# Optimization experiments

Measured on AMD Instinct MI355X. Metric: run time of the kernel, lower is better.

Reference implementation:

```python
import jax, jax.numpy as jnp
import numpy as np

THRESH = 0.59275  # PercolationQ default threshold
SIZES = list(range(3, 42, 2))  # 20 Chebyshev scales
B, P, C = 16, 100, 3


def _connected_components(imgs):
    # imgs: (N, s, s) int32 in {0,1}. 4-connectivity CC via min-label propagation.
    # Label value = (min flat index in component) + 1, background = 0.
    N, s, _ = imgs.shape
    big = s * s + 1
    fg = imgs > 0
    idx = jnp.arange(s * s, dtype=jnp.int32).reshape(1, s, s) + 1
    init = jnp.where(fg, idx, big)

    def body(state):
        L, _ = state
        Lp = jnp.pad(L, ((0, 0), (1, 1), (1, 1)), constant_values=big)
        m = jnp.minimum(jnp.minimum(Lp[:, :-2, 1:-1], Lp[:, 2:, 1:-1]),
                        jnp.minimum(Lp[:, 1:-1, :-2], Lp[:, 1:-1, 2:]))
        Ln = jnp.where(fg, jnp.minimum(L, m), big)
        return Ln, jnp.any(Ln != L)

    L, _ = jax.lax.while_loop(lambda st: st[1], body, (init, jnp.bool_(True)))
    return jnp.where(fg, L, 0)


def _scale_features(x):
    b, p, s, _, c = x.shape
    # --- Chebyshev layer (faithful to the TF reshape + center-crop semantics) ---
    r = x.reshape(b * s, p, s, c)
    center = r[:, (p - 1) // 2, (s - 1) // 2, :][:, None, None, :]
    binm = (jnp.abs(r - center).max(axis=3) <= float(s)).astype(jnp.int32).reshape(b, p, s, s)
    # --- Probability: histogram of per-patch foreground counts ---
    counts = binm.sum(axis=(2, 3))  # (b, p), values in [0, s^2]
    L = s * s + 1
    hist = jax.vmap(lambda cc: jnp.bincount(cc, length=L))(counts).astype(jnp.float32) / p
    numbers = jnp.concatenate([jnp.ones((1,), jnp.float32), jnp.arange(1, L, dtype=jnp.float32)])
    # --- FractalDimension / Lacunarity ---
    fd = (hist / numbers).sum(axis=1)
    mu1 = (hist * numbers).sum(axis=1) ** 2
    mu2 = (hist * numbers ** 2).sum(axis=1)
    lac = (mu2 - mu1) / mu1
    # --- PercolationQ ---
    pq = ((counts.astype(jnp.float32) / (s * s)) >= THRESH).astype(jnp.float32).mean(axis=1)
    # --- Clusterize (tfa semantics: labels unique/consecutive across the whole batch) ---
    labels = _connected_components(binm.reshape(b * p, s, s))
    lhist = jax.vmap(lambda l: jnp.bincount(l.ravel(), length=L))(labels)  # (b*p, s^2+1)
    ncomp = (lhist[:, 1:] > 0).sum(axis=1)
    # max global label in image i = cumulative component count (0 if no components)
    maxlab = jnp.where(ncomp > 0, jnp.cumsum(ncomp), 0)
    pc = maxlab.astype(jnp.float32).reshape(b, p).mean(axis=1)
    # PercolationM: max bincount over per-sample flattened global labels
    #   = max(total background pixels, largest component size in the sample)
    bg = lhist[:, 0].reshape(b, p).sum(axis=1)
    maxcomp = lhist[:, 1:].max(axis=1).reshape(b, p).max(axis=1)
    pm = jnp.maximum(bg, maxcomp).astype(jnp.float32)
    return fd, lac, pq, pc, pm


def _forward(xs):
    feats = [_scale_features(x) for x in xs]
    fd = jnp.stack([f[0] for f in feats], axis=1)
    lac = jnp.stack([f[1] for f in feats], axis=1)
    pq = jnp.stack([f[2] for f in feats], axis=1)
    pc = jnp.stack([f[3] for f in feats], axis=1)
    pm = jnp.stack([f[4] for f in feats], axis=1)
    out = jnp.concatenate([pc, pq, pm, lac, fd], axis=1)  # (B, 100)
    return out.reshape(-1, 10, 10)


def setup_inputs() -> dict:
    key = jax.random.key(0)
    inp = {}
    for i, s in enumerate(SIZES):
        inp[f"x{i}"] = jax.random.normal(jax.random.fold_in(key, i), (B, P, s, s, C), dtype=jnp.float32)
    return inp


def reference(x0, x1, x2, x3, x4, x5, x6, x7, x8, x9, x10, x11, x12, x13, x14, x15, x16, x17, x18, x19):
    return _forward([x0, x1, x2, x3, x4, x5, x6, x7, x8, x9, x10, x11, x12, x13, x14, x15, x16, x17, x18, x19])
```

## Files before the change

kernel.cpp:

```cpp
#include <hip/hip_runtime.h>

#define NSCALES 20
#define PATCH 100
#define IMGS_PER_SCALE 1600
#define TOTAL_IMGS 32000
#define THREADS 256
#define PXT 16
#define CHUNKPX (THREADS * PXT)
#define MAXIMG 464
#define S2MAX 1681

struct Ptrs   { const float* p[NSCALES]; };
struct Starts { int blkStart[NSCALES]; };

template<int S>
__device__ __forceinline__ void count_body(const float* __restrict__ x,
                                           int blkLocal, int sc,
                                           int* __restrict__ wsC2,
                                           float4* cenL, int* cntL)
{
    constexpr int S2 = S * S;
    constexpr int ROWDIV = 100 * S;
    const int Ntot = IMGS_PER_SCALE * S2;
    const int P0   = blkLocal * CHUNKPX;
    const int Pend = min(P0 + CHUNKPX, Ntot);
    const int tid  = threadIdx.x;

    const int imgBase = P0 / S2;
    const int imgLast = (Pend - 1) / S2;
    const int nImg    = imgLast - imgBase + 1;
    const int j0      = P0 / ROWDIV;
    const int jEnd    = (Pend - 1) / ROWDIV;
    const int nj      = jEnd - j0 + 1;

    if (tid < nj) {
        int j = j0 + tid;
        const float* c = x + (size_t)(((j * PATCH + 49) * S + (S >> 1)) * 3);
        cenL[tid] = make_float4(c[0], c[1], c[2], 0.f);
    }
    for (int t = tid; t < nImg; t += THREADS) cntL[t] = 0;
    __syncthreads();

    const int p0 = P0 + tid * PXT;
    if (p0 < Pend) {
        const float4* q4 = (const float4*)(x + (size_t)p0 * 3);
        float4 v[12];
        #pragma unroll
        for (int q = 0; q < 12; q++) v[q] = q4[q];
        const float* f = (const float*)v;

        const int iA = p0 / S2;
        const int r0 = p0 - iA * S2;
        const int jA = p0 / ROWDIV;
        const int jB = (p0 + PXT - 1) / ROWDIV;
        const float4 ceA = cenL[jA - j0];
        const float4 ceB = (jB != jA) ? cenL[jB - j0] : ceA;
        const int flip = (jB != jA) ? ((jA + 1) * ROWDIV - p0) : PXT;

        int cA = 0, cB = 0, cC = 0;
        #pragma unroll
        for (int q = 0; q < PXT; q++) {
            const float4 ce = (q < flip) ? ceA : ceB;
            float d = fmaxf(fmaxf(fabsf(f[q*3+0] - ce.x),
                                  fabsf(f[q*3+1] - ce.y)),
                            fabsf(f[q*3+2] - ce.z));
            int fg = (d <= (float)S) ? 1 : 0;
            int t  = r0 + q;
            if constexpr (S2 >= PXT) {
                cA += (t < S2) ? fg : 0;
                cB += (t >= S2) ? fg : 0;
            } else {
                cA += (t < S2) ? fg : 0;
                cB += (t >= S2 && t < 2 * S2) ? fg : 0;
                cC += (t >= 2 * S2) ? fg : 0;
            }
        }
        atomicAdd(&cntL[iA - imgBase], cA);
        if (cB) atomicAdd(&cntL[iA + 1 - imgBase], cB);
        if constexpr (S2 < PXT) {
            if (cC) atomicAdd(&cntL[iA + 2 - imgBase], cC);
        }
    }
    __syncthreads();

    for (int t = tid; t < nImg; t += THREADS) {
        int img = imgBase + t;
        int lo = img * S2, hi = lo + S2;
        int g = sc * IMGS_PER_SCALE + img;
        int vv = cntL[t];
        if (lo >= P0) {
            wsC2[2 * g] = vv;
            if (hi <= Pend) wsC2[2 * g + 1] = 0;
        } else {
            wsC2[2 * g + 1] = vv;
        }
    }
}

__global__ __launch_bounds__(THREADS)
void count_kernel(Ptrs ptrs, Starts st, int* __restrict__ wsC2)
{
    const int bid = blockIdx.x;
    int sc = 0;
    #pragma unroll
    for (int k = 1; k < NSCALES; k++) sc += (bid >= st.blkStart[k]) ? 1 : 0;
    const int blkLocal = bid - st.blkStart[sc];

    __shared__ float4 cenL[16];
    __shared__ int    cntL[MAXIMG];

    switch (sc) {
#define CASE(i) case i: count_body<3 + 2*(i)>(ptrs.p[i], blkLocal, i, wsC2, cenL, cntL); break;
        CASE(0)  CASE(1)  CASE(2)  CASE(3)  CASE(4)
        CASE(5)  CASE(6)  CASE(7)  CASE(8)  CASE(9)
        CASE(10) CASE(11) CASE(12) CASE(13) CASE(14)
        CASE(15) CASE(16) CASE(17) CASE(18) CASE(19)
#undef CASE
    }
}

__global__ __launch_bounds__(THREADS)
void cc_kernel(Ptrs ptrs, const int* __restrict__ wsC2,
               int* __restrict__ wsCnt,
               int* __restrict__ wsNcomp, int* __restrict__ wsMaxc)
{
    const int bid = blockIdx.x;
    const int sc  = bid / 25;
    const int s   = 3 + 2 * sc;
    const int s2  = s * s;
    const int BIGL = s2 + 1;
    const float* __restrict__ x = ptrs.p[sc];
    const int imgLoc0 = (bid % 25) * 64;
    const int tid = threadIdx.x;
    const unsigned mS = 0xFFFFFFFFu / (unsigned)s + 1;

    __shared__ int slowList[64];
    __shared__ int nslow;
    __shared__ int lab[S2MAX];
    __shared__ int szh[S2MAX];
    __shared__ int redN[4], redM[4];

    if (tid == 0) nslow = 0;
    __syncthreads();
    if (tid < 64) {
        int img = imgLoc0 + tid;
        int g = sc * IMGS_PER_SCALE + img;
        int c = wsC2[2 * g] + wsC2[2 * g + 1];
        wsCnt[g] = c;
        if (c == s2)      { wsNcomp[g] = 1; wsMaxc[g] = s2; }
        else if (c == 0)  { wsNcomp[g] = 0; wsMaxc[g] = 0; }
        else { int k = atomicAdd(&nslow, 1); slowList[k] = img; }
    }
    __syncthreads();
    const int ns = nslow;
    if (ns == 0) return;

    if (s2 <= 64) {
        const int w = tid >> 6, l = tid & 63;
        for (int idx = w; idx < ns; idx += 4) {
            int img = slowList[idx];
            int fg = 0, labr = BIGL, i1 = 0, i2 = 0;
            if (l < s2) {
                i1 = (int)__umulhi((unsigned)l, mS);
                i2 = l - i1 * s;
                int M = img * s + i1;
                int j = M / PATCH;
                const float* ce = x + (size_t)(((j * PATCH + 49) * s + (s >> 1)) * 3);
                const float* px = x + ((size_t)img * s2 + l) * 3;
                float d = fmaxf(fmaxf(fabsf(px[0] - ce[0]), fabsf(px[1] - ce[1])),
                                fabsf(px[2] - ce[2]));
                if (d <= (float)s) { fg = 1; labr = l + 1; }
            }
            for (;;) {
                int m = labr;
                int vU = __shfl(labr, (l - s) & 63);
                int vD = __shfl(labr, (l + s) & 63);
                int vL = __shfl(labr, (l - 1) & 63);
                int vR = __shfl(labr, (l + 1) & 63);
                if (fg) {
                    if (i1 > 0)     m = min(m, vU);
                    if (i1 < s - 1) m = min(m, vD);
                    if (i2 > 0)     m = min(m, vL);
                    if (i2 < s - 1) m = min(m, vR);
                }
                int vJ = __shfl(labr, (m - 1) & 63);
                if (fg) m = min(m, vJ);
                unsigned long long chg = __ballot(m < labr);
                labr = m;
                if (chg == 0) break;
            }
            int ncomp = __popcll(__ballot(fg && labr == l + 1));
            int mc = 0;
            for (int r = 0; r < s2; r++) {
                int szr = __popcll(__ballot(fg && labr == r + 1));
                mc = max(mc, szr);
            }
            if (l == 0) {
                int g = sc * IMGS_PER_SCALE + img;
                wsNcomp[g] = ncomp; wsMaxc[g] = mc;
            }
        }
    } else {
        for (int idx = 0; idx < ns; idx++) {
            int img = slowList[idx];
            const int ibase = img * s2 * 3;
            for (int i = tid; i < s2; i += THREADS) {
                int i1 = (int)__umulhi((unsigned)i, mS);
                int M = img * s + i1;
                int j = M / PATCH;
                const float* ce = x + (size_t)(((j * PATCH + 49) * s + (s >> 1)) * 3);
                const float* px = x + ibase + i * 3;
                float d = fmaxf(fmaxf(fabsf(px[0] - ce[0]), fabsf(px[1] - ce[1])),
                                fabsf(px[2] - ce[2]));
                lab[i] = (d <= (float)s) ? (i + 1) : BIGL;
                szh[i] = 0;
            }
            __syncthreads();
            for (;;) {
                bool changed = false;
                for (int i = tid; i < s2; i += THREADS) {
                    int L0 = lab[i];
                    if (L0 <= s2) {
                        int i1 = (int)__umulhi((unsigned)i, mS);
                        int i2 = i - i1 * s;
                        int m = L0;
                        if (i1 > 0)     m = min(m, lab[i - s]);
                        if (i1 < s - 1) m = min(m, lab[i + s]);
                        if (i2 > 0)     m = min(m, lab[i - 1]);
                        if (i2 < s - 1) m = min(m, lab[i + 1]);
                        m = min(m, lab[m - 1]);
                        if (m < L0) { lab[i] = m; changed = true; }
                    }
                }
                if (__syncthreads_count(changed ? 1 : 0) == 0) break;
            }
            int ncomp = 0;
            for (int i = tid; i < s2; i += THREADS) {
                int L = lab[i];
                if (L <= s2) {
                    atomicAdd(&szh[L - 1], 1);
                    if (L == i + 1) ncomp++;
                }
            }
            __syncthreads();
            int mc = 0;
            for (int i = tid; i < s2; i += THREADS) mc = max(mc, szh[i]);
            for (int m = 32; m >= 1; m >>= 1) {
                ncomp += __shfl_xor(ncomp, m);
                mc     = max(mc, __shfl_xor(mc, m));
            }
            int wid = tid >> 6, lane = tid & 63;
            if (lane == 0) { redN[wid] = ncomp; redM[wid] = mc; }
            __syncthreads();
            if (tid == 0) {
                int g = sc * IMGS_PER_SCALE + img;
                wsNcomp[g] = redN[0] + redN[1] + redN[2] + redN[3];
                wsMaxc[g]  = max(max(redM[0], redM[1]), max(redM[2], redM[3]));
            }
            __syncthreads();
        }
    }
}

__global__ __launch_bounds__(THREADS)
void final_kernel(const int* __restrict__ wsCnt,
                  const int* __restrict__ wsNcomp,
                  const int* __restrict__ wsMaxc,
                  float* __restrict__ out)
{
    const int scale = blockIdx.x;
    const int s  = 3 + 2 * scale;
    const int s2 = s * s;
    const int tid = threadIdx.x;
    const int NB = IMGS_PER_SCALE;
    const int CH = 7;

    __shared__ int nc[IMGS_PER_SCALE];
    __shared__ int tsum[THREADS];

    for (int i = tid; i < NB; i += THREADS) nc[i] = wsNcomp[scale * NB + i];
    __syncthreads();

    int lsum = 0;
    for (int k = 0; k < CH; k++) {
        int idx = tid * CH + k;
        if (idx < NB) lsum += nc[idx];
    }
    tsum[tid] = lsum;
    __syncthreads();
    for (int st = 1; st < THREADS; st <<= 1) {
        int v = (tid >= st) ? tsum[tid - st] : 0;
        __syncthreads();
        tsum[tid] += v;
        __syncthreads();
    }
    int run = (tid > 0) ? tsum[tid - 1] : 0;
    for (int k = 0; k < CH; k++) {
        int idx = tid * CH + k;
        if (idx < NB) {
            int v = nc[idx];
            run += v;
            nc[idx] = (v > 0) ? run : 0;
        }
    }
    __syncthreads();

    int b    = tid >> 4;
    int lane = tid & 15;
    float fdsum = 0.f, sn = 0.f, sn2 = 0.f, pcsum = 0.f;
    int pqc = 0, bg = 0, mcx = 0;
    for (int q = lane; q < PATCH; q += 16) {
        int i = b * PATCH + q;
        int c = wsCnt[scale * NB + i];
        float n = (c > 0) ? (float)c : 1.0f;
        fdsum += 1.0f / n;
        sn    += n;
        sn2   += n * n;
        pqc   += ((float)c / (float)s2 >= 0.59275f) ? 1 : 0;
        bg    += (s2 - c);
        mcx    = max(mcx, wsMaxc[scale * NB + i]);
        pcsum += (float)nc[i];
    }
    for (int m = 8; m >= 1; m >>= 1) {
        fdsum += __shfl_xor(fdsum, m);
        sn    += __shfl_xor(sn, m);
        sn2   += __shfl_xor(sn2, m);
        pcsum += __shfl_xor(pcsum, m);
        pqc   += __shfl_xor(pqc, m);
        bg    += __shfl_xor(bg, m);
        mcx    = max(mcx, __shfl_xor(mcx, m));
    }
    if (lane == 0) {
        float fd  = fdsum / 100.0f;
        float m1  = sn / 100.0f;
        float mu1 = m1 * m1;
        float mu2 = sn2 / 100.0f;
        float lac = (mu2 - mu1) / mu1;
        float pq  = (float)pqc / 100.0f;
        float pc  = pcsum / 100.0f;
        float pm  = (float)max(bg, mcx);
        out[b * 100 +  0 + scale] = pc;
        out[b * 100 + 20 + scale] = pq;
        out[b * 100 + 40 + scale] = pm;
        out[b * 100 + 60 + scale] = lac;
        out[b * 100 + 80 + scale] = fd;
    }
}

extern "C" void kernel_launch(void* const* d_in, const int* in_sizes, int n_in,
                              void* d_out, int out_size, void* d_ws, size_t ws_size,
                              hipStream_t stream)
{
    Ptrs ptrs;
    for (int i = 0; i < NSCALES; i++) ptrs.p[i] = (const float*)d_in[i];

    Starts st;
    int acc = 0;
    for (int i = 0; i < NSCALES; i++) {
        st.blkStart[i] = acc;
        int s = 3 + 2 * i, s2 = s * s;
        acc += (IMGS_PER_SCALE * s2 + CHUNKPX - 1) / CHUNKPX;
    }

    int* wsC2  = (int*)d_ws;
    int* wsCnt = wsC2 + 2 * TOTAL_IMGS;
    int* wsN   = wsCnt + TOTAL_IMGS;
    int* wsM   = wsN + TOTAL_IMGS;

    count_kernel<<<acc, THREADS, 0, stream>>>(ptrs, st, wsC2);
    cc_kernel<<<TOTAL_IMGS / 64, THREADS, 0, stream>>>(ptrs, wsC2, wsCnt, wsN, wsM);
    final_kernel<<<NSCALES, THREADS, 0, stream>>>(wsCnt, wsN, wsM, (float*)d_out);
}
```

Baseline: 67.68 us.

## Stage count-kernel input through LDS with coalesced float4 loads and smaller chunks

The count kernel now has each thread load float4s in a coalesced, thread-interleaved pattern into a shared-memory staging buffer. Each thread then reads 4 pixels twice from shared memory, replacing the old scheme where a thread read 12 contiguous float4s directly from global memory. The chunk per block is halved to 2048 pixels, which doubles the block count and shrinks the per-block image count buffer. The aim is better global memory coalescing and more parallelism, at the cost of 24KB of LDS per block, an extra staging pass and more per-block overhead.

Measured after the change: 67.63 us. About the same (-0.1%).

```diff
diff --git a/kernel.cpp b/kernel.cpp
--- a/kernel.cpp
+++ b/kernel.cpp
@@ -5,9 +5,10 @@
 #define IMGS_PER_SCALE 1600
 #define TOTAL_IMGS 32000
 #define THREADS 256
-#define PXT 16
-#define CHUNKPX (THREADS * PXT)
-#define MAXIMG 464
+#define CHUNKPX 2048
+#define NF4BLK (CHUNKPX * 3 / 4)
+#define F4PT (NF4BLK / THREADS)
+#define MAXIMG 240
 #define S2MAX 1681
 
 struct Ptrs   { const float* p[NSCALES]; };
@@ -17,14 +18,16 @@
 __device__ __forceinline__ void count_body(const float* __restrict__ x,
                                            int blkLocal, int sc,
                                            int* __restrict__ wsC2,
-                                           float4* cenL, int* cntL)
+                                           float4* stgF4, float4* cenL,
+                                           int* cntL)
 {
     constexpr int S2 = S * S;
     constexpr int ROWDIV = 100 * S;
-    const int Ntot = IMGS_PER_SCALE * S2;
-    const int P0   = blkLocal * CHUNKPX;
-    const int Pend = min(P0 + CHUNKPX, Ntot);
-    const int tid  = threadIdx.x;
+    const int Ntot   = IMGS_PER_SCALE * S2;
+    const int NF4tot = Ntot * 3 / 4;
+    const int P0     = blkLocal * CHUNKPX;
+    const int Pend   = min(P0 + CHUNKPX, Ntot);
+    const int tid    = threadIdx.x;
 
     const int imgBase = P0 / S2;
     const int imgLast = (Pend - 1) / S2;
@@ -33,52 +36,55 @@
     const int jEnd    = (Pend - 1) / ROWDIV;
     const int nj      = jEnd - j0 + 1;
 
+    const float4* __restrict__ x4 = (const float4*)x;
+    const int F0 = blkLocal * NF4BLK;
+    float4 stg[F4PT];
+    #pragma unroll
+    for (int it = 0; it < F4PT; it++) {
+        int fi = F0 + it * THREADS + tid;
+        stg[it] = x4[min(fi, NF4tot - 1)];
+    }
     if (tid < nj) {
         int j = j0 + tid;
         const float* c = x + (size_t)(((j * PATCH + 49) * S + (S >> 1)) * 3);
         cenL[tid] = make_float4(c[0], c[1], c[2], 0.f);
     }
     for (int t = tid; t < nImg; t += THREADS) cntL[t] = 0;
-    __syncthreads();
-
-    const int p0 = P0 + tid * PXT;
-    if (p0 < Pend) {
-        const float4* q4 = (const float4*)(x + (size_t)p0 * 3);
-        float4 v[12];
-        #pragma unroll
-        for (int q = 0; q < 12; q++) v[q] = q4[q];
-        const float* f = (const float*)v;
-
-        const int iA = p0 / S2;
-        const int r0 = p0 - iA * S2;
-        const int jA = p0 / ROWDIV;
-        const int jB = (p0 + PXT - 1) / ROWDIV;
-        const float4 ceA = cenL[jA - j0];
-        const float4 ceB = (jB != jA) ? cenL[jB - j0] : ceA;
-        const int flip = (jB != jA) ? ((jA + 1) * ROWDIV - p0) : PXT;
-
-        int cA = 0, cB = 0, cC = 0;
-        #pragma unroll
-        for (int q = 0; q < PXT; q++) {
-            const float4 ce = (q < flip) ? ceA : ceB;
-            float d = fmaxf(fmaxf(fabsf(f[q*3+0] - ce.x),
-                                  fabsf(f[q*3+1] - ce.y)),
-                            fabsf(f[q*3+2] - ce.z));
-            int fg = (d <= (float)S) ? 1 : 0;
-            int t  = r0 + q;
-            if constexpr (S2 >= PXT) {
+    #pragma unroll
+    for (int it = 0; it < F4PT; it++) stgF4[it * THREADS + tid] = stg[it];
+    __syncthreads();
+
+    const float* lf = (const float*)stgF4;
+    #pragma unroll
+    for (int half = 0; half < 2; half++) {
+        const int p0 = P0 + half * (CHUNKPX / 2) + tid * 4;
+        if (p0 < Pend) {
+            const float4* src = (const float4*)(lf + (size_t)(p0 - P0) * 3);
+            float4 a = src[0], b = src[1], c = src[2];
+            const float f[12] = {a.x,a.y,a.z,a.w, b.x,b.y,b.z,b.w,
+                                 c.x,c.y,c.z,c.w};
+            const int iA = p0 / S2;
+            const int r0 = p0 - iA * S2;
+            const int jA = p0 / ROWDIV;
+            const int jB = (p0 + 3) / ROWDIV;
+            const float4 ceA = cenL[jA - j0];
+            const float4 ceB = (jB != jA) ? cenL[jB - j0] : ceA;
+            const int flip = (jB != jA) ? ((jA + 1) * ROWDIV - p0) : 4;
+
+            int cA = 0, cB = 0;
+            #pragma unroll
+            for (int q = 0; q < 4; q++) {
+                const float4 ce = (q < flip) ? ceA : ceB;
+                float d = fmaxf(fmaxf(fabsf(f[q*3+0] - ce.x),
+                                      fabsf(f[q*3+1] - ce.y)),
+                                fabsf(f[q*3+2] - ce.z));
+                int fg = (d <= (float)S) ? 1 : 0;
+                int t  = r0 + q;
                 cA += (t < S2) ? fg : 0;
                 cB += (t >= S2) ? fg : 0;
-            } else {
-                cA += (t < S2) ? fg : 0;
-                cB += (t >= S2 && t < 2 * S2) ? fg : 0;
-                cC += (t >= 2 * S2) ? fg : 0;
-            }
-        }
-        atomicAdd(&cntL[iA - imgBase], cA);
-        if (cB) atomicAdd(&cntL[iA + 1 - imgBase], cB);
-        if constexpr (S2 < PXT) {
-            if (cC) atomicAdd(&cntL[iA + 2 - imgBase], cC);
+            }
+            atomicAdd(&cntL[iA - imgBase], cA);
+            if (cB) atomicAdd(&cntL[iA + 1 - imgBase], cB);
         }
     }
     __syncthreads();
@@ -106,11 +112,12 @@
     for (int k = 1; k < NSCALES; k++) sc += (bid >= st.blkStart[k]) ? 1 : 0;
     const int blkLocal = bid - st.blkStart[sc];
 
-    __shared__ float4 cenL[16];
+    __shared__ float4 stgF4[NF4BLK];
+    __shared__ float4 cenL[8];
     __shared__ int    cntL[MAXIMG];
 
     switch (sc) {
-#define CASE(i) case i: count_body<3 + 2*(i)>(ptrs.p[i], blkLocal, i, wsC2, cenL, cntL); break;
+#define CASE(i) case i: count_body<3 + 2*(i)>(ptrs.p[i], blkLocal, i, wsC2, stgF4, cenL, cntL); break;
         CASE(0)  CASE(1)  CASE(2)  CASE(3)  CASE(4)
         CASE(5)  CASE(6)  CASE(7)  CASE(8)  CASE(9)
         CASE(10) CASE(11) CASE(12) CASE(13) CASE(14)
```

## Count background pixels with strided loads and sparse global atomics

Applied to the files above, without the earlier changes.

The count kernel now has each thread read pixels strided by the block size instead of a contiguous 16-pixel run. Each pixel's patch-center value is loaded directly from global memory rather than staged in shared memory. Only background pixels are counted, via global atomics into a zeroed per-image array, and foreground count is recovered as s² minus that. This removes shared-memory setup, two barriers and the two-part per-image count handoff. In exchange it adds a memset launch, scalar uncoalesced 3-float loads, and possibly many global atomics if background is common.

New measurement: 70.40 us. 4.0% more time.

```diff
diff --git a/kernel.cpp b/kernel.cpp
--- a/kernel.cpp
+++ b/kernel.cpp
@@ -5,112 +5,63 @@
 #define IMGS_PER_SCALE 1600
 #define TOTAL_IMGS 32000
 #define THREADS 256
-#define PXT 16
+#define PXT 8
 #define CHUNKPX (THREADS * PXT)
-#define MAXIMG 464
 #define S2MAX 1681
 
 struct Ptrs   { const float* p[NSCALES]; };
-struct Starts { int blkStart[NSCALES]; };
+struct Starts { int chunkStart[NSCALES]; };
 
 template<int S>
-__device__ __forceinline__ void count_body(const float* __restrict__ x,
-                                           int blkLocal, int sc,
-                                           int* __restrict__ wsC2,
-                                           float4* cenL, int* cntL)
+__device__ __forceinline__ void count_chunk(const float* __restrict__ x,
+                                            int chunkLocal, int sc,
+                                            int* __restrict__ bgCnt)
 {
     constexpr int S2 = S * S;
     constexpr int ROWDIV = 100 * S;
     const int Ntot = IMGS_PER_SCALE * S2;
-    const int P0   = blkLocal * CHUNKPX;
-    const int Pend = min(P0 + CHUNKPX, Ntot);
-    const int tid  = threadIdx.x;
-
-    const int imgBase = P0 / S2;
-    const int imgLast = (Pend - 1) / S2;
-    const int nImg    = imgLast - imgBase + 1;
-    const int j0      = P0 / ROWDIV;
-    const int jEnd    = (Pend - 1) / ROWDIV;
-    const int nj      = jEnd - j0 + 1;
-
-    if (tid < nj) {
-        int j = j0 + tid;
+    const int P0   = chunkLocal * CHUNKPX + (int)threadIdx.x;
+
+    float p0[PXT], p1[PXT], p2[PXT];
+    float c0[PXT], c1[PXT], c2[PXT];
+    #pragma unroll
+    for (int i = 0; i < PXT; i++) {
+        const int Pc = min(P0 + i * THREADS, Ntot - 1);
+        const float* p = x + (size_t)Pc * 3;
+        p0[i] = p[0]; p1[i] = p[1]; p2[i] = p[2];
+        const int j = Pc / ROWDIV;
         const float* c = x + (size_t)(((j * PATCH + 49) * S + (S >> 1)) * 3);
-        cenL[tid] = make_float4(c[0], c[1], c[2], 0.f);
-    }
-    for (int t = tid; t < nImg; t += THREADS) cntL[t] = 0;
-    __syncthreads();
-
-    const int p0 = P0 + tid * PXT;
-    if (p0 < Pend) {
-        const float4* q4 = (const float4*)(x + (size_t)p0 * 3);
-        float4 v[12];
+        c0[i] = c[0]; c1[i] = c[1]; c2[i] = c[2];
+    }
+    unsigned bgm = 0;
+    #pragma unroll
+    for (int i = 0; i < PXT; i++) {
+        float d = fmaxf(fmaxf(fabsf(p0[i] - c0[i]), fabsf(p1[i] - c1[i])),
+                        fabsf(p2[i] - c2[i]));
+        if (d > (float)S && (P0 + i * THREADS) < Ntot) bgm |= 1u << i;
+    }
+    if (bgm) {
         #pragma unroll
-        for (int q = 0; q < 12; q++) v[q] = q4[q];
-        const float* f = (const float*)v;
-
-        const int iA = p0 / S2;
-        const int r0 = p0 - iA * S2;
-        const int jA = p0 / ROWDIV;
-        const int jB = (p0 + PXT - 1) / ROWDIV;
-        const float4 ceA = cenL[jA - j0];
-        const float4 ceB = (jB != jA) ? cenL[jB - j0] : ceA;
-        const int flip = (jB != jA) ? ((jA + 1) * ROWDIV - p0) : PXT;
-
-        int cA = 0, cB = 0, cC = 0;
-        #pragma unroll
-        for (int q = 0; q < PXT; q++) {
-            const float4 ce = (q < flip) ? ceA : ceB;
-            float d = fmaxf(fmaxf(fabsf(f[q*3+0] - ce.x),
-                                  fabsf(f[q*3+1] - ce.y)),
-                            fabsf(f[q*3+2] - ce.z));
-            int fg = (d <= (float)S) ? 1 : 0;
-            int t  = r0 + q;
-            if constexpr (S2 >= PXT) {
-                cA += (t < S2) ? fg : 0;
-                cB += (t >= S2) ? fg : 0;
-            } else {
-                cA += (t < S2) ? fg : 0;
-                cB += (t >= S2 && t < 2 * S2) ? fg : 0;
-                cC += (t >= 2 * S2) ? fg : 0;
+        for (int i = 0; i < PXT; i++) {
+            if (bgm & (1u << i)) {
+                int img = (P0 + i * THREADS) / S2;
+                atomicAdd(&bgCnt[sc * IMGS_PER_SCALE + img], 1);
             }
         }
-        atomicAdd(&cntL[iA - imgBase], cA);
-        if (cB) atomicAdd(&cntL[iA + 1 - imgBase], cB);
-        if constexpr (S2 < PXT) {
-            if (cC) atomicAdd(&cntL[iA + 2 - imgBase], cC);
-        }
-    }
-    __syncthreads();
-
-    for (int t = tid; t < nImg; t += THREADS) {
-        int img = imgBase + t;
-        int lo = img * S2, hi = lo + S2;
-        int g = sc * IMGS_PER_SCALE + img;
-        int vv = cntL[t];
-        if (lo >= P0) {
-            wsC2[2 * g] = vv;
-            if (hi <= Pend) wsC2[2 * g + 1] = 0;
-        } else {
-            wsC2[2 * g + 1] = vv;
-        }
     }
 }
 
 __global__ __launch_bounds__(THREADS)
-void count_kernel(Ptrs ptrs, Starts st, int* __restrict__ wsC2)
+void count_kernel(Ptrs ptrs, Starts st, int* __restrict__ bgCnt)
 {
     const int bid = blockIdx.x;
     int sc = 0;
     #pragma unroll
-    for (int k = 1; k < NSCALES; k++) sc += (bid >= st.blkStart[k]) ? 1 : 0;
-    const int blkLocal = bid - st.blkStart[sc];
-
-    __shared__ float4 cenL[16];
-    __shared__ int    cntL[MAXIMG];
+    for (int k = 1; k < NSCALES; k++) sc += (bid >= st.chunkStart[k]) ? 1 : 0;
+    const int cl = bid - st.chunkStart[sc];
 
     switch (sc) {
-#define CASE(i) case i: count_body<3 + 2*(i)>(ptrs.p[i], blkLocal, i, wsC2, cenL, cntL); break;
+#define CASE(i) case i: count_chunk<3 + 2*(i)>(ptrs.p[i], cl, i, bgCnt); break;
         CASE(0)  CASE(1)  CASE(2)  CASE(3)  CASE(4)
         CASE(5)  CASE(6)  CASE(7)  CASE(8)  CASE(9)
         CASE(10) CASE(11) CASE(12) CASE(13) CASE(14)
@@ -120,7 +71,7 @@
 }
 
 __global__ __launch_bounds__(THREADS)
-void cc_kernel(Ptrs ptrs, const int* __restrict__ wsC2,
+void cc_kernel(Ptrs ptrs, const int* __restrict__ bgCnt,
                int* __restrict__ wsCnt,
                int* __restrict__ wsNcomp, int* __restrict__ wsMaxc)
 {
@@ -145,7 +96,7 @@
     if (tid < 64) {
         int img = imgLoc0 + tid;
         int g = sc * IMGS_PER_SCALE + img;
-        int c = wsC2[2 * g] + wsC2[2 * g + 1];
+        int c = s2 - bgCnt[g];
         wsCnt[g] = c;
         if (c == s2)      { wsNcomp[g] = 1; wsMaxc[g] = s2; }
         else if (c == 0)  { wsNcomp[g] = 0; wsMaxc[g] = 0; }
@@ -357,17 +308,18 @@
     Starts st;
     int acc = 0;
     for (int i = 0; i < NSCALES; i++) {
-        st.blkStart[i] = acc;
+        st.chunkStart[i] = acc;
         int s = 3 + 2 * i, s2 = s * s;
         acc += (IMGS_PER_SCALE * s2 + CHUNKPX - 1) / CHUNKPX;
     }
 
-    int* wsC2  = (int*)d_ws;
-    int* wsCnt = wsC2 + 2 * TOTAL_IMGS;
+    int* bgCnt = (int*)d_ws;
+    int* wsCnt = bgCnt + TOTAL_IMGS;
     int* wsN   = wsCnt + TOTAL_IMGS;
     int* wsM   = wsN + TOTAL_IMGS;
 
-    count_kernel<<<acc, THREADS, 0, stream>>>(ptrs, st, wsC2);
-    cc_kernel<<<TOTAL_IMGS / 64, THREADS, 0, stream>>>(ptrs, wsC2, wsCnt, wsN, wsM);
+    hipMemsetAsync(bgCnt, 0, TOTAL_IMGS * sizeof(int), stream);
+    count_kernel<<<acc, THREADS, 0, stream>>>(ptrs, st, bgCnt);
+    cc_kernel<<<TOTAL_IMGS / 64, THREADS, 0, stream>>>(ptrs, bgCnt, wsCnt, wsN, wsM);
     final_kernel<<<NSCALES, THREADS, 0, stream>>>(wsCnt, wsN, wsM, (float*)d_out);
 }
```
